# Optimization experiments

Measured on AMD Instinct MI355X. Metric: run time of the kernel, lower is better.

Reference implementation:

```python
import jax, jax.numpy as jnp
import numpy as np

B, S, H = 2, 2048, 2048
NH = 16
HD = H // NH  # 128


def setup_inputs() -> dict:
    key = jax.random.key(0)
    ks = jax.random.split(key, 6)
    sc = 0.02
    return {
        "x": jax.random.normal(ks[0], (B, S, H), dtype=jnp.float32),
        "attention_mask": jnp.zeros((B, S), dtype=jnp.float32),
        "Wq": jax.random.normal(ks[1], (H, H), dtype=jnp.float32) * sc,
        "bq": jnp.zeros((H,), dtype=jnp.float32),
        "Wk": jax.random.normal(ks[2], (H, H), dtype=jnp.float32) * sc,
        "bk": jnp.zeros((H,), dtype=jnp.float32),
        "Wv": jax.random.normal(ks[3], (H, H), dtype=jnp.float32) * sc,
        "bv": jnp.zeros((H,), dtype=jnp.float32),
        "Wo": jax.random.normal(ks[4], (H, H), dtype=jnp.float32) * sc,
        "bo": jnp.zeros((H,), dtype=jnp.float32),
    }


def reference(x, attention_mask, Wq, bq, Wk, bk, Wv, bv, Wo, bo):
    b, s, h = x.shape
    q = (x @ Wq + bq).reshape(b, s, NH, HD)
    k = (x @ Wk + bk).reshape(b, s, NH, HD)
    v = (x @ Wv + bv).reshape(b, s, NH, HD)
    scale = 1.0 / jnp.sqrt(jnp.asarray(HD, dtype=x.dtype))
    scores = jnp.einsum('bqhd,bkhd->bhqk', q, k) * scale
    scores = scores + attention_mask[:, None, None, :]
    weights = jax.nn.softmax(scores, axis=-1)
    attn = jnp.einsum('bhqk,bkhd->bqhd', weights, v).reshape(b, s, h)
    return attn @ Wo + bo
```

## Files before the change

kernel.cpp:

```cpp
#include <hip/hip_runtime.h>
#include <hip/hip_bf16.h>
#include <stdint.h>

#define BB   2
#define SS   2048
#define HHH  2048
#define NHH  16
#define HDD  128
#define MTOT 4096

typedef __bf16 bf16x8 __attribute__((ext_vector_type(8)));
typedef float  f32x4  __attribute__((ext_vector_type(4)));
typedef float  f32x16 __attribute__((ext_vector_type(16)));

#define MFMA16(a, b, c) __builtin_amdgcn_mfma_f32_16x16x32_bf16((a), (b), (c), 0, 0, 0)
#define MFMA32(a, b, c) __builtin_amdgcn_mfma_f32_32x32x16_bf16((a), (b), (c), 0, 0, 0)

__device__ __forceinline__ unsigned short f2bf(float f) {
    union { float f; unsigned u; } v; v.f = f;
    unsigned r = v.u + 0x7FFFu + ((v.u >> 16) & 1u);
    return (unsigned short)(r >> 16);
}

__device__ __forceinline__ unsigned packbf(float a, float b) {
    union { __bf16 h[2]; unsigned u; } p;
    p.h[0] = (__bf16)a; p.h[1] = (__bf16)b;
    return p.u;
}

__device__ __forceinline__ void pswap(unsigned &a, unsigned &b) {
    asm("v_permlane32_swap_b32 %0, %1" : "+v"(a), "+v"(b));
}

__device__ __forceinline__ float2 xswap(float x) {
    unsigned a = __builtin_bit_cast(unsigned, x);
    unsigned b;
    asm("v_mov_b32 %0, %1" : "=v"(b) : "v"(a));
    asm("v_permlane32_swap_b32 %0, %1" : "+v"(a), "+v"(b));
    return make_float2(__builtin_bit_cast(float, a), __builtin_bit_cast(float, b));
}

__device__ __forceinline__ void gload16(const void* src, void* lds) {
    __builtin_amdgcn_global_load_lds(
        (__attribute__((address_space(1))) void*)src,
        (__attribute__((address_space(3))) void*)lds,
        16, 0, 0);
}

__global__ void cast_f32_bf16(const float* __restrict__ in,
                              unsigned short* __restrict__ out, int n) {
    int i = (blockIdx.x * blockDim.x + threadIdx.x) * 4;
    int stride = gridDim.x * blockDim.x * 4;
    for (; i < n; i += stride) {
        float4 v = *(const float4*)(in + i);
        ushort4 o;
        o.x = f2bf(v.x); o.y = f2bf(v.y); o.z = f2bf(v.z); o.w = f2bf(v.w);
        *(ushort4*)(out + i) = o;
    }
}

__global__ void transpose_cast4(const float* __restrict__ W0, const float* __restrict__ W1,
                                const float* __restrict__ W2, const float* __restrict__ W3,
                                unsigned short* __restrict__ out) {
    const float* in = blockIdx.z == 0 ? W0 : blockIdx.z == 1 ? W1 : blockIdx.z == 2 ? W2 : W3;
    unsigned short* o = out + (size_t)blockIdx.z * ((size_t)HHH * HHH);
    __shared__ float tile[32][33];
    int c0 = blockIdx.x * 32, r0 = blockIdx.y * 32;
    int tx = threadIdx.x, ty = threadIdx.y;
    #pragma unroll
    for (int i = 0; i < 32; i += 8)
        tile[ty + i][tx] = in[(size_t)(r0 + ty + i) * HHH + c0 + tx];
    __syncthreads();
    #pragma unroll
    for (int i = 0; i < 32; i += 8)
        o[(size_t)(c0 + ty + i) * HHH + r0 + tx] = f2bf(tile[tx][ty + i]);
}

template<int MODE>
__global__ __launch_bounds__(512, 2) void gemm8_bf16(
    const unsigned short* __restrict__ A,
    const unsigned short* __restrict__ Bt,
    const float* __restrict__ bias,
    void* __restrict__ Cout,
    int M, int N, int K)
{
    __shared__ __align__(16) unsigned char sm[147456];
    const int tid = threadIdx.x;
    const int wv = tid >> 6, ln = tid & 63;
    const int g = ln >> 4, r = ln & 15;
    const int wr = wv >> 2, wc = wv & 3;

    const int bid = blockIdx.x;
    const int lb = (bid & 7) * 32 + (bid >> 3);
    const int m0 = (lb & 31) * 128;
    const int n0 = (lb >> 5) * 256;

    unsigned srcA[2]; int ldsA[2];
    #pragma unroll
    for (int j = 0; j < 2; ++j) {
        int o = j * 8192 + tid * 16;
        int row = o >> 7;
        int lg = ((o >> 4) & 7) ^ (row & 7);
        srcA[j] = (unsigned)(m0 + row) * K + lg * 8;
        ldsA[j] = o;
    }
    unsigned srcB[4]; int ldsB[4];
    #pragma unroll
    for (int j = 0; j < 4; ++j) {
        int o = j * 8192 + tid * 16;
        int row = o >> 7;
        int lg = ((o >> 4) & 7) ^ (row & 7);
        srcB[j] = (unsigned)(n0 + row) * K + lg * 8;
        ldsB[j] = 16384 + o;
    }

    f32x4 acc[4][4];
    #pragma unroll
    for (int i = 0; i < 4; ++i)
        #pragma unroll
        for (int j = 0; j < 4; ++j)
            acc[i][j] = (f32x4){0.f, 0.f, 0.f, 0.f};

    const int NT = K >> 6;

    {
        unsigned char* b0 = sm;
        unsigned char* b1 = sm + 49152;
        #pragma unroll
        for (int j = 0; j < 2; ++j) gload16(A + srcA[j], b0 + ldsA[j]);
        #pragma unroll
        for (int j = 0; j < 4; ++j) gload16(Bt + srcB[j], b0 + ldsB[j]);
        #pragma unroll
        for (int j = 0; j < 2; ++j) gload16(A + srcA[j] + 64, b1 + ldsA[j]);
        #pragma unroll
        for (int j = 0; j < 4; ++j) gload16(Bt + srcB[j] + 64, b1 + ldsB[j]);
    }
    asm volatile("s_waitcnt vmcnt(6)" ::: "memory");
    __builtin_amdgcn_s_barrier();

    int csel = 0;
    int psel = 2;
    for (int t = 0; t < NT; ++t) {
        const unsigned char* Ab = sm + csel * 49152;
        const unsigned char* Bb = Ab + 16384;
        unsigned char* Pb = sm + psel * 49152;
        const bool pre = (t + 2 < NT);
        const int ko = (t + 2) * 64;

        bf16x8 af[2][2], bf[2][2];
        #define LDA(mi, ks) (*(const bf16x8*)(Ab + (wr * 64 + (mi) * 16 + r) * 128 + \
                             ((((ks) << 2) + g) ^ ((wr * 64 + (mi) * 16 + r) & 7)) * 16))
        #define LDB(ni, ks) (*(const bf16x8*)(Bb + (wc * 64 + (ni) * 16 + r) * 128 + \
                             ((((ks) << 2) + g) ^ ((wc * 64 + (ni) * 16 + r) & 7)) * 16))

        af[0][0] = LDA(0, 0); af[0][1] = LDA(0, 1);
        af[1][0] = LDA(1, 0); af[1][1] = LDA(1, 1);
        bf[0][0] = LDB(0, 0); bf[0][1] = LDB(0, 1);
        bf[1][0] = LDB(1, 0); bf[1][1] = LDB(1, 1);
        if (pre) { gload16(Bt + srcB[0] + ko, Pb + ldsB[0]);
                   gload16(Bt + srcB[1] + ko, Pb + ldsB[1]); }
        __builtin_amdgcn_s_barrier();
        asm volatile("s_waitcnt lgkmcnt(0)" ::: "memory");
        __builtin_amdgcn_s_setprio(1);
        #pragma unroll
        for (int mi = 0; mi < 2; ++mi)
            #pragma unroll
            for (int ni = 0; ni < 2; ++ni)
                #pragma unroll
                for (int ks = 0; ks < 2; ++ks)
                    acc[mi][ni] = MFMA16(af[mi][ks], bf[ni][ks], acc[mi][ni]);
        __builtin_amdgcn_s_setprio(0);
        __builtin_amdgcn_s_barrier();

        bf[0][0] = LDB(2, 0); bf[0][1] = LDB(2, 1);
        bf[1][0] = LDB(3, 0); bf[1][1] = LDB(3, 1);
        if (pre) { gload16(Bt + srcB[2] + ko, Pb + ldsB[2]);
                   gload16(Bt + srcB[3] + ko, Pb + ldsB[3]); }
        __builtin_amdgcn_s_barrier();
        asm volatile("s_waitcnt lgkmcnt(0)" ::: "memory");
        __builtin_amdgcn_s_setprio(1);
        #pragma unroll
        for (int mi = 0; mi < 2; ++mi)
            #pragma unroll
            for (int ni = 0; ni < 2; ++ni)
                #pragma unroll
                for (int ks = 0; ks < 2; ++ks)
                    acc[mi][ni + 2] = MFMA16(af[mi][ks], bf[ni][ks], acc[mi][ni + 2]);
        __builtin_amdgcn_s_setprio(0);
        __builtin_amdgcn_s_barrier();

        af[0][0] = LDA(2, 0); af[0][1] = LDA(2, 1);
        af[1][0] = LDA(3, 0); af[1][1] = LDA(3, 1);
        if (pre) { gload16(A + srcA[0] + ko, Pb + ldsA[0]);
                   gload16(A + srcA[1] + ko, Pb + ldsA[1]); }
        __builtin_amdgcn_s_barrier();
        asm volatile("s_waitcnt lgkmcnt(0)" ::: "memory");
        __builtin_amdgcn_s_setprio(1);
        #pragma unroll
        for (int mi = 0; mi < 2; ++mi)
            #pragma unroll
            for (int ni = 0; ni < 2; ++ni)
                #pragma unroll
                for (int ks = 0; ks < 2; ++ks)
                    acc[mi + 2][ni + 2] = MFMA16(af[mi][ks], bf[ni][ks], acc[mi + 2][ni + 2]);
        __builtin_amdgcn_s_setprio(0);
        __builtin_amdgcn_s_barrier();

        bf[0][0] = LDB(0, 0); bf[0][1] = LDB(0, 1);
        bf[1][0] = LDB(1, 0); bf[1][1] = LDB(1, 1);
        __builtin_amdgcn_s_barrier();
        asm volatile("s_waitcnt lgkmcnt(0)" ::: "memory");
        __builtin_amdgcn_s_setprio(1);
        #pragma unroll
        for (int mi = 0; mi < 2; ++mi)
            #pragma unroll
            for (int ni = 0; ni < 2; ++ni)
                #pragma unroll
                for (int ks = 0; ks < 2; ++ks)
                    acc[mi + 2][ni] = MFMA16(af[mi][ks], bf[ni][ks], acc[mi + 2][ni]);
        __builtin_amdgcn_s_setprio(0);
        __builtin_amdgcn_s_barrier();

        if (pre) asm volatile("s_waitcnt vmcnt(6)" ::: "memory");
        else     asm volatile("s_waitcnt vmcnt(0)" ::: "memory");
        __builtin_amdgcn_s_barrier();

        csel = (csel == 2) ? 0 : csel + 1;
        psel = (psel == 2) ? 0 : psel + 1;
        #undef LDA
        #undef LDB
    }

    #pragma unroll
    for (int mt = 0; mt < 4; ++mt) {
        #pragma unroll
        for (int nt = 0; nt < 4; ++nt) {
            int col = n0 + wc * 64 + nt * 16 + r;
            float bvv = bias[col];
            f32x4 a = acc[mt][nt];
            int mrow = m0 + wr * 64 + mt * 16 + g * 4;
            if (MODE == 0) {
                #pragma unroll
                for (int q = 0; q < 4; ++q)
                    ((unsigned short*)Cout)[(size_t)(mrow + q) * N + col] = f2bf(a[q] + bvv);
            } else if (MODE == 2) {
                #pragma unroll
                for (int q = 0; q < 4; ++q)
                    ((float*)Cout)[(size_t)(mrow + q) * N + col] = a[q] + bvv;
            } else {
                int b = mrow >> 11, s0x = mrow & 2047;
                ushort4 o;
                o.x = f2bf(a[0] + bvv); o.y = f2bf(a[1] + bvv);
                o.z = f2bf(a[2] + bvv); o.w = f2bf(a[3] + bvv);
                *(ushort4*)((unsigned short*)Cout + ((size_t)(b * 2048 + col)) * 2048 + s0x) = o;
            }
        }
    }
}

__global__ __launch_bounds__(256, 2) void attn_fwd(
    const unsigned short* __restrict__ Q,
    const unsigned short* __restrict__ K,
    const unsigned short* __restrict__ V,
    const float* __restrict__ mask,
    unsigned short* __restrict__ O)
{
    __shared__ __align__(16) unsigned char sm[65536];
    const int tid = threadIdx.x, wv = tid >> 6, ln = tid & 63;
    const int hi = ln >> 5, qr = ln & 31;

    const int bid = blockIdx.x;
    const int lb = (bid & 7) * 64 + (bid >> 3);
    const int qb = lb & 15;
    const int bh = lb >> 4;
    const int h = bh & 15, b = bh >> 4;

    const size_t rowQ0 = (size_t)(b * 2048 + qb * 128 + wv * 32);
    const float SCL2 = 0.08838834764831845f * 1.4426950408889634f;
    const float L2E  = 1.4426950408889634f;

    unsigned srcK[4], srcV[4];
    int ldsK[4], ldsV[4];
    #pragma unroll
    for (int i = 0; i < 4; ++i) {
        int ch = wv * 4 + i;
        int o = ch * 1024 + ln * 16;
        { int row = o >> 8; int gl = ((o >> 4) & 15) ^ (row & 7);
          srcK[i] = (unsigned)((b * 2048 + row) * 2048 + h * 128 + gl * 8);
          ldsK[i] = ch * 1024; }
        { int d = o >> 7; int gl = ((o >> 4) & 7) ^ (d & 7);
          srcV[i] = (unsigned)((b * 2048 + h * 128 + d) * 2048 + gl * 8);
          ldsV[i] = 16384 + ch * 1024; }
    }

    #pragma unroll
    for (int i = 0; i < 4; ++i) {
        gload16(K + srcK[i], sm + ldsK[i]);
        gload16(V + srcV[i], sm + ldsV[i]);
    }

    bf16x8 qf[8];
    #pragma unroll
    for (int ks = 0; ks < 8; ++ks)
        qf[ks] = *(const bf16x8*)(Q + (rowQ0 + qr) * 2048 + h * 128 + ks * 16 + hi * 8);

    f32x16 acc[4];
    #pragma unroll
    for (int i = 0; i < 4; ++i)
        #pragma unroll
        for (int j = 0; j < 16; ++j)
            acc[i][j] = 0.f;
    float mr = -3.0e38f, lr = 0.f;

    const float* mb = mask + b * 2048;
    int cur = 0;
    __syncthreads();

    for (int kb = 0; kb < SS; kb += 64) {
        if (kb + 64 < SS) {
            const unsigned char* dst = sm + (cur ^ 1) * 32768;
            int ko = (kb + 64) * 2048;
            #pragma unroll
            for (int i = 0; i < 4; ++i) {
                gload16(K + srcK[i] + ko, (void*)(dst + ldsK[i]));
                gload16(V + srcV[i] + (kb + 64), (void*)(dst + ldsV[i]));
            }
        }
        const unsigned char* Kt = sm + cur * 32768;
        const unsigned char* Vt = Kt + 16384;

        f32x4 mk[2][4];
        #pragma unroll
        for (int kb2 = 0; kb2 < 2; ++kb2)
            #pragma unroll
            for (int rg = 0; rg < 4; ++rg)
                mk[kb2][rg] = *(const f32x4*)(mb + kb + kb2 * 32 + rg * 8 + hi * 4);

        f32x16 sf0, sf1;
        #pragma unroll
        for (int j = 0; j < 16; ++j) { sf0[j] = 0.f; sf1[j] = 0.f; }
        __builtin_amdgcn_s_setprio(1);
        #pragma unroll
        for (int ks = 0; ks < 8; ++ks) {
            int row0 = qr, row1 = 32 + qr;
            int s0 = ((2 * ks + hi) ^ (row0 & 7));
            int s1 = ((2 * ks + hi) ^ (row1 & 7));
            bf16x8 kf0 = *(const bf16x8*)(Kt + row0 * 256 + s0 * 16);
            bf16x8 kf1 = *(const bf16x8*)(Kt + row1 * 256 + s1 * 16);
            sf0 = MFMA32(kf0, qf[ks], sf0);
            sf1 = MFMA32(kf1, qf[ks], sf1);
        }
        __builtin_amdgcn_s_setprio(0);

        float sv[2][16];
        #pragma unroll
        for (int reg = 0; reg < 16; ++reg) {
            sv[0][reg] = sf0[reg] * SCL2 + mk[0][reg >> 2][reg & 3] * L2E;
            sv[1][reg] = sf1[reg] * SCL2 + mk[1][reg >> 2][reg & 3] * L2E;
        }

        float mx[8];
        #pragma unroll
        for (int j = 0; j < 8; ++j)
            mx[j] = fmaxf(fmaxf(sv[0][2*j], sv[0][2*j+1]),
                          fmaxf(sv[1][2*j], sv[1][2*j+1]));
        float m01 = fmaxf(fmaxf(fmaxf(mx[0], mx[1]), fmaxf(mx[2], mx[3])),
                          fmaxf(fmaxf(mx[4], mx[5]), fmaxf(mx[6], mx[7])));
        float2 mp = xswap(m01);
        float mt = fmaxf(mp.x, mp.y);

        float alpha = 1.f;
        int allskip = __all(mt <= mr + 8.f);
        if (!allskip) {
            float nm = fmaxf(mr, mt);
            alpha = __builtin_amdgcn_exp2f(mr - nm);
            mr = nm;
            #pragma unroll
            for (int dblk = 0; dblk < 4; ++dblk)
                #pragma unroll
                for (int reg = 0; reg < 16; ++reg)
                    acc[dblk][reg] *= alpha;
        }

        float s0 = 0.f, s1 = 0.f, s2 = 0.f, s3 = 0.f;
        #pragma unroll
        for (int kb2 = 0; kb2 < 2; ++kb2)
            #pragma unroll
            for (int reg = 0; reg < 16; reg += 4) {
                float p0 = __builtin_amdgcn_exp2f(sv[kb2][reg + 0] - mr);
                float p1 = __builtin_amdgcn_exp2f(sv[kb2][reg + 1] - mr);
                float p2 = __builtin_amdgcn_exp2f(sv[kb2][reg + 2] - mr);
                float p3 = __builtin_amdgcn_exp2f(sv[kb2][reg + 3] - mr);
                sv[kb2][reg + 0] = p0; sv[kb2][reg + 1] = p1;
                sv[kb2][reg + 2] = p2; sv[kb2][reg + 3] = p3;
                s0 += p0; s1 += p1; s2 += p2; s3 += p3;
            }
        float rsl = (s0 + s1) + (s2 + s3);
        float2 rp = xswap(rsl);
        float rs = rp.x + rp.y;
        lr = lr * alpha + rs;

        bf16x8 pfr[4];
        #pragma unroll
        for (int kb16 = 0; kb16 < 4; ++kb16) {
            const int kb2 = kb16 >> 1, i2 = kb16 & 1;
            float* pv = sv[kb2];
            unsigned W00 = packbf(pv[(2*i2+0)*4 + 0], pv[(2*i2+0)*4 + 1]);
            unsigned W01 = packbf(pv[(2*i2+0)*4 + 2], pv[(2*i2+0)*4 + 3]);
            unsigned W10 = packbf(pv[(2*i2+1)*4 + 0], pv[(2*i2+1)*4 + 1]);
            unsigned W11 = packbf(pv[(2*i2+1)*4 + 2], pv[(2*i2+1)*4 + 3]);
            pswap(W00, W10);
            pswap(W01, W11);
            union { unsigned w[4]; bf16x8 v; } u;
            u.w[0] = W00; u.w[1] = W01; u.w[2] = W10; u.w[3] = W11;
            pfr[kb16] = u.v;
        }

        __builtin_amdgcn_s_setprio(1);
        #pragma unroll
        for (int dblk = 0; dblk < 4; ++dblk) {
            int d = dblk * 32 + qr;
            f32x16 a = acc[dblk];
            #pragma unroll
            for (int kb16 = 0; kb16 < 4; ++kb16) {
                int s = ((2 * kb16 + hi) ^ (d & 7));
                bf16x8 vf = *(const bf16x8*)(Vt + d * 128 + s * 16);
                a = MFMA32(vf, pfr[kb16], a);
            }
            acc[dblk] = a;
        }
        __builtin_amdgcn_s_setprio(0);

        __syncthreads();
        cur ^= 1;
    }

    float linv = 1.f / lr;
    unsigned short* orow = O + (rowQ0 + qr) * 2048 + h * 128;
    #pragma unroll
    for (int dblk = 0; dblk < 4; ++dblk)
        #pragma unroll
        for (int rg = 0; rg < 4; ++rg) {
            float v0 = acc[dblk][rg * 4 + 0] * linv;
            float v1 = acc[dblk][rg * 4 + 1] * linv;
            float v2 = acc[dblk][rg * 4 + 2] * linv;
            float v3 = acc[dblk][rg * 4 + 3] * linv;
            uint2 o;
            o.x = packbf(v0, v1);
            o.y = packbf(v2, v3);
            *(uint2*)(orow + dblk * 32 + rg * 8 + hi * 4) = o;
        }
}

extern "C" void kernel_launch(void* const* d_in, const int* in_sizes, int n_in,
                              void* d_out, int out_size, void* d_ws, size_t ws_size,
                              hipStream_t stream)
{
    (void)in_sizes; (void)n_in; (void)out_size; (void)ws_size;
    const float* x    = (const float*)d_in[0];
    const float* mask = (const float*)d_in[1];
    const float* Wq   = (const float*)d_in[2];
    const float* bq   = (const float*)d_in[3];
    const float* Wk   = (const float*)d_in[4];
    const float* bk   = (const float*)d_in[5];
    const float* Wv   = (const float*)d_in[6];
    const float* bv   = (const float*)d_in[7];
    const float* Wo   = (const float*)d_in[8];
    const float* bo   = (const float*)d_in[9];
    float* out = (float*)d_out;

    char* ws = (char*)d_ws;
    unsigned short* xb  = (unsigned short*)(ws);
    unsigned short* Wqt = (unsigned short*)(ws + (16u << 20));
    unsigned short* Wkt = (unsigned short*)(ws + (24u << 20));
    unsigned short* Wvt = (unsigned short*)(ws + (32u << 20));
    unsigned short* Wot = (unsigned short*)(ws + (40u << 20));
    unsigned short* Qb  = (unsigned short*)(ws + (48u << 20));
    unsigned short* Kb  = (unsigned short*)(ws + (64u << 20));
    unsigned short* Vtb = (unsigned short*)(ws + (80u << 20));
    unsigned short* Ab  = (unsigned short*)(ws + (16u << 20));

    cast_f32_bf16<<<2048, 256, 0, stream>>>(x, xb, MTOT * HHH);
    transpose_cast4<<<dim3(64, 64, 4), dim3(32, 8), 0, stream>>>(Wq, Wk, Wv, Wo, Wqt);

    gemm8_bf16<0><<<256, 512, 0, stream>>>(xb, Wqt, bq, Qb,  MTOT, HHH, HHH);
    gemm8_bf16<0><<<256, 512, 0, stream>>>(xb, Wkt, bk, Kb,  MTOT, HHH, HHH);
    gemm8_bf16<1><<<256, 512, 0, stream>>>(xb, Wvt, bv, Vtb, MTOT, HHH, HHH);

    attn_fwd<<<BB * NHH * (SS / 128), 256, 0, stream>>>(Qb, Kb, Vtb, mask, Ab);

    gemm8_bf16<2><<<256, 512, 0, stream>>>(Ab, Wot, bo, out, MTOT, HHH, HHH);
}
```

Measured before the change: 290.6 us.

## Split attention KV range across two blocks and merge partials in combine kernel

Splits the attention over keys into two halves (split-K / flash-decoding style). Each half is handled by its own block with smaller 32-key tiles and half the LDS, which allows higher occupancy via launch bounds of 4. Each block writes a normalized partial output plus its running max and sum. A new combine kernel then rescales and merges the two partials into the final attention output. This targets low occupancy and too few blocks in the attention kernel, at the cost of extra partial-output traffic, an added launch, and a second bf16 rounding step.

```diff
diff --git a/kernel.cpp b/kernel.cpp
--- a/kernel.cpp
+++ b/kernel.cpp
@@ -45,6 +45,13 @@
         (__attribute__((address_space(1))) void*)src,
         (__attribute__((address_space(3))) void*)lds,
         16, 0, 0);
+}
+
+__device__ __forceinline__ float bflo(unsigned w) {
+    return __builtin_bit_cast(float, w << 16);
+}
+__device__ __forceinline__ float bfhi(unsigned w) {
+    return __builtin_bit_cast(float, w & 0xffff0000u);
 }
 
 __global__ void cast_f32_bf16(const float* __restrict__ in,
@@ -258,43 +265,48 @@
     }
 }
 
-__global__ __launch_bounds__(256, 2) void attn_fwd(
+__global__ __launch_bounds__(256, 4) void attn_fwd(
     const unsigned short* __restrict__ Q,
     const unsigned short* __restrict__ K,
     const unsigned short* __restrict__ V,
     const float* __restrict__ mask,
-    unsigned short* __restrict__ O)
+    unsigned short* __restrict__ P0,
+    unsigned short* __restrict__ P1,
+    float2* __restrict__ ML0,
+    float2* __restrict__ ML1)
 {
-    __shared__ __align__(16) unsigned char sm[65536];
+    __shared__ __align__(16) unsigned char sm[32768];
     const int tid = threadIdx.x, wv = tid >> 6, ln = tid & 63;
     const int hi = ln >> 5, qr = ln & 31;
 
     const int bid = blockIdx.x;
-    const int lb = (bid & 7) * 64 + (bid >> 3);
-    const int qb = lb & 15;
-    const int bh = lb >> 4;
+    const int lb = (bid & 7) * 128 + (bid >> 3);
+    const int sp = lb & 1;
+    const int qb = (lb >> 1) & 15;
+    const int bh = lb >> 5;
     const int h = bh & 15, b = bh >> 4;
 
     const size_t rowQ0 = (size_t)(b * 2048 + qb * 128 + wv * 32);
+    const int kbase = sp * 1024;
     const float SCL2 = 0.08838834764831845f * 1.4426950408889634f;
     const float L2E  = 1.4426950408889634f;
 
-    unsigned srcK[4], srcV[4];
-    int ldsK[4], ldsV[4];
-    #pragma unroll
-    for (int i = 0; i < 4; ++i) {
-        int ch = wv * 4 + i;
+    unsigned srcK[2], srcV[2];
+    int ldsK[2], ldsV[2];
+    #pragma unroll
+    for (int i = 0; i < 2; ++i) {
+        int ch = wv * 2 + i;
         int o = ch * 1024 + ln * 16;
         { int row = o >> 8; int gl = ((o >> 4) & 15) ^ (row & 7);
-          srcK[i] = (unsigned)((b * 2048 + row) * 2048 + h * 128 + gl * 8);
-          ldsK[i] = ch * 1024; }
-        { int d = o >> 7; int gl = ((o >> 4) & 7) ^ (d & 7);
-          srcV[i] = (unsigned)((b * 2048 + h * 128 + d) * 2048 + gl * 8);
-          ldsV[i] = 16384 + ch * 1024; }
-    }
-
-    #pragma unroll
-    for (int i = 0; i < 4; ++i) {
+          srcK[i] = (unsigned)((b * 2048 + kbase + row) * 2048 + h * 128 + gl * 8);
+          ldsK[i] = o; }
+        { int d = o >> 6; int gl = ((o >> 4) & 3) ^ (d & 3);
+          srcV[i] = (unsigned)((b * 2048 + h * 128 + d) * 2048 + kbase + gl * 8);
+          ldsV[i] = 8192 + o; }
+    }
+
+    #pragma unroll
+    for (int i = 0; i < 2; ++i) {
         gload16(K + srcK[i], sm + ldsK[i]);
         gload16(V + srcV[i], sm + ldsV[i]);
     }
@@ -312,58 +324,49 @@
             acc[i][j] = 0.f;
     float mr = -3.0e38f, lr = 0.f;
 
-    const float* mb = mask + b * 2048;
+    const float* mb = mask + b * 2048 + kbase;
     int cur = 0;
     __syncthreads();
 
-    for (int kb = 0; kb < SS; kb += 64) {
-        if (kb + 64 < SS) {
-            const unsigned char* dst = sm + (cur ^ 1) * 32768;
-            int ko = (kb + 64) * 2048;
-            #pragma unroll
-            for (int i = 0; i < 4; ++i) {
-                gload16(K + srcK[i] + ko, (void*)(dst + ldsK[i]));
-                gload16(V + srcV[i] + (kb + 64), (void*)(dst + ldsV[i]));
+    for (int t = 0; t < 32; ++t) {
+        const int kb = t * 32;
+        if (t + 1 < 32) {
+            unsigned char* dst = sm + (cur ^ 1) * 16384;
+            #pragma unroll
+            for (int i = 0; i < 2; ++i) {
+                gload16(K + srcK[i] + (kb + 32) * 2048, dst + ldsK[i]);
+                gload16(V + srcV[i] + (kb + 32), dst + ldsV[i]);
             }
         }
-        const unsigned char* Kt = sm + cur * 32768;
-        const unsigned char* Vt = Kt + 16384;
-
-        f32x4 mk[2][4];
-        #pragma unroll
-        for (int kb2 = 0; kb2 < 2; ++kb2)
-            #pragma unroll
-            for (int rg = 0; rg < 4; ++rg)
-                mk[kb2][rg] = *(const f32x4*)(mb + kb + kb2 * 32 + rg * 8 + hi * 4);
-
-        f32x16 sf0, sf1;
-        #pragma unroll
-        for (int j = 0; j < 16; ++j) { sf0[j] = 0.f; sf1[j] = 0.f; }
+        const unsigned char* Kt = sm + cur * 16384;
+        const unsigned char* Vt = Kt + 8192;
+
+        f32x4 mk[4];
+        #pragma unroll
+        for (int rg = 0; rg < 4; ++rg)
+            mk[rg] = *(const f32x4*)(mb + kb + rg * 8 + hi * 4);
+
+        f32x16 sf;
+        #pragma unroll
+        for (int j = 0; j < 16; ++j) sf[j] = 0.f;
         __builtin_amdgcn_s_setprio(1);
         #pragma unroll
         for (int ks = 0; ks < 8; ++ks) {
-            int row0 = qr, row1 = 32 + qr;
-            int s0 = ((2 * ks + hi) ^ (row0 & 7));
-            int s1 = ((2 * ks + hi) ^ (row1 & 7));
-            bf16x8 kf0 = *(const bf16x8*)(Kt + row0 * 256 + s0 * 16);
-            bf16x8 kf1 = *(const bf16x8*)(Kt + row1 * 256 + s1 * 16);
-            sf0 = MFMA32(kf0, qf[ks], sf0);
-            sf1 = MFMA32(kf1, qf[ks], sf1);
+            int s0 = (2 * ks + hi) ^ (qr & 7);
+            bf16x8 kf = *(const bf16x8*)(Kt + qr * 256 + s0 * 16);
+            sf = MFMA32(kf, qf[ks], sf);
         }
         __builtin_amdgcn_s_setprio(0);
 
-        float sv[2][16];
-        #pragma unroll
-        for (int reg = 0; reg < 16; ++reg) {
-            sv[0][reg] = sf0[reg] * SCL2 + mk[0][reg >> 2][reg & 3] * L2E;
-            sv[1][reg] = sf1[reg] * SCL2 + mk[1][reg >> 2][reg & 3] * L2E;
-        }
+        float sv[16];
+        #pragma unroll
+        for (int reg = 0; reg < 16; ++reg)
+            sv[reg] = sf[reg] * SCL2 + mk[reg >> 2][reg & 3] * L2E;
 
         float mx[8];
         #pragma unroll
         for (int j = 0; j < 8; ++j)
-            mx[j] = fmaxf(fmaxf(sv[0][2*j], sv[0][2*j+1]),
-                          fmaxf(sv[1][2*j], sv[1][2*j+1]));
+            mx[j] = fmaxf(sv[2 * j], sv[2 * j + 1]);
         float m01 = fmaxf(fmaxf(fmaxf(mx[0], mx[1]), fmaxf(mx[2], mx[3])),
                           fmaxf(fmaxf(mx[4], mx[5]), fmaxf(mx[6], mx[7])));
         float2 mp = xswap(m01);
@@ -384,31 +387,27 @@
 
         float s0 = 0.f, s1 = 0.f, s2 = 0.f, s3 = 0.f;
         #pragma unroll
-        for (int kb2 = 0; kb2 < 2; ++kb2)
-            #pragma unroll
-            for (int reg = 0; reg < 16; reg += 4) {
-                float p0 = __builtin_amdgcn_exp2f(sv[kb2][reg + 0] - mr);
-                float p1 = __builtin_amdgcn_exp2f(sv[kb2][reg + 1] - mr);
-                float p2 = __builtin_amdgcn_exp2f(sv[kb2][reg + 2] - mr);
-                float p3 = __builtin_amdgcn_exp2f(sv[kb2][reg + 3] - mr);
-                sv[kb2][reg + 0] = p0; sv[kb2][reg + 1] = p1;
-                sv[kb2][reg + 2] = p2; sv[kb2][reg + 3] = p3;
-                s0 += p0; s1 += p1; s2 += p2; s3 += p3;
-            }
+        for (int reg = 0; reg < 16; reg += 4) {
+            float p0 = __builtin_amdgcn_exp2f(sv[reg + 0] - mr);
+            float p1 = __builtin_amdgcn_exp2f(sv[reg + 1] - mr);
+            float p2 = __builtin_amdgcn_exp2f(sv[reg + 2] - mr);
+            float p3 = __builtin_amdgcn_exp2f(sv[reg + 3] - mr);
+            sv[reg + 0] = p0; sv[reg + 1] = p1;
+            sv[reg + 2] = p2; sv[reg + 3] = p3;
+            s0 += p0; s1 += p1; s2 += p2; s3 += p3;
+        }
         float rsl = (s0 + s1) + (s2 + s3);
         float2 rp = xswap(rsl);
         float rs = rp.x + rp.y;
         lr = lr * alpha + rs;
 
-        bf16x8 pfr[4];
-        #pragma unroll
-        for (int kb16 = 0; kb16 < 4; ++kb16) {
-            const int kb2 = kb16 >> 1, i2 = kb16 & 1;
-            float* pv = sv[kb2];
-            unsigned W00 = packbf(pv[(2*i2+0)*4 + 0], pv[(2*i2+0)*4 + 1]);
-            unsigned W01 = packbf(pv[(2*i2+0)*4 + 2], pv[(2*i2+0)*4 + 3]);
-            unsigned W10 = packbf(pv[(2*i2+1)*4 + 0], pv[(2*i2+1)*4 + 1]);
-            unsigned W11 = packbf(pv[(2*i2+1)*4 + 2], pv[(2*i2+1)*4 + 3]);
+        bf16x8 pfr[2];
+        #pragma unroll
+        for (int kb16 = 0; kb16 < 2; ++kb16) {
+            unsigned W00 = packbf(sv[(2*kb16+0)*4 + 0], sv[(2*kb16+0)*4 + 1]);
+            unsigned W01 = packbf(sv[(2*kb16+0)*4 + 2], sv[(2*kb16+0)*4 + 3]);
+            unsigned W10 = packbf(sv[(2*kb16+1)*4 + 0], sv[(2*kb16+1)*4 + 1]);
+            unsigned W11 = packbf(sv[(2*kb16+1)*4 + 2], sv[(2*kb16+1)*4 + 3]);
             pswap(W00, W10);
             pswap(W01, W11);
             union { unsigned w[4]; bf16x8 v; } u;
@@ -422,9 +421,9 @@
             int d = dblk * 32 + qr;
             f32x16 a = acc[dblk];
             #pragma unroll
-            for (int kb16 = 0; kb16 < 4; ++kb16) {
-                int s = ((2 * kb16 + hi) ^ (d & 7));
-                bf16x8 vf = *(const bf16x8*)(Vt + d * 128 + s * 16);
+            for (int kb16 = 0; kb16 < 2; ++kb16) {
+                int s = (2 * kb16 + hi) ^ (d & 3);
+                bf16x8 vf = *(const bf16x8*)(Vt + d * 64 + s * 16);
                 a = MFMA32(vf, pfr[kb16], a);
             }
             acc[dblk] = a;
@@ -436,7 +435,8 @@
     }
 
     float linv = 1.f / lr;
-    unsigned short* orow = O + (rowQ0 + qr) * 2048 + h * 128;
+    unsigned short* Pp = sp ? P1 : P0;
+    unsigned short* orow = Pp + (rowQ0 + qr) * 2048 + h * 128;
     #pragma unroll
     for (int dblk = 0; dblk < 4; ++dblk)
         #pragma unroll
@@ -450,6 +450,37 @@
             o.y = packbf(v2, v3);
             *(uint2*)(orow + dblk * 32 + rg * 8 + hi * 4) = o;
         }
+    if (hi == 0) {
+        float2* ml = sp ? ML1 : ML0;
+        ml[(rowQ0 + qr) * 16 + h] = make_float2(mr, lr);
+    }
+}
+
+__global__ void attn_combine(const unsigned short* __restrict__ P0,
+                             const unsigned short* __restrict__ P1,
+                             const float2* __restrict__ ML0,
+                             const float2* __restrict__ ML1,
+                             unsigned short* __restrict__ O)
+{
+    int t = blockIdx.x * 256 + threadIdx.x;
+    int base = t * 8;
+    int row = base >> 11;
+    int h = (base & 2047) >> 7;
+    float2 a = ML0[row * 16 + h];
+    float2 c = ML1[row * 16 + h];
+    float M = fmaxf(a.x, c.x);
+    float w0 = __builtin_amdgcn_exp2f(a.x - M) * a.y;
+    float w1 = __builtin_amdgcn_exp2f(c.x - M) * c.y;
+    float inv = 1.f / (w0 + w1);
+    w0 *= inv; w1 *= inv;
+    uint4 u0 = *(const uint4*)(P0 + base);
+    uint4 u1 = *(const uint4*)(P1 + base);
+    uint4 o;
+    o.x = packbf(w0 * bflo(u0.x) + w1 * bflo(u1.x), w0 * bfhi(u0.x) + w1 * bfhi(u1.x));
+    o.y = packbf(w0 * bflo(u0.y) + w1 * bflo(u1.y), w0 * bfhi(u0.y) + w1 * bfhi(u1.y));
+    o.z = packbf(w0 * bflo(u0.z) + w1 * bflo(u1.z), w0 * bfhi(u0.z) + w1 * bfhi(u1.z));
+    o.w = packbf(w0 * bflo(u0.w) + w1 * bflo(u1.w), w0 * bfhi(u0.w) + w1 * bfhi(u1.w));
+    *(uint4*)(O + base) = o;
 }
 
 extern "C" void kernel_launch(void* const* d_in, const int* in_sizes, int n_in,
@@ -478,7 +509,11 @@
     unsigned short* Qb  = (unsigned short*)(ws + (48u << 20));
     unsigned short* Kb  = (unsigned short*)(ws + (64u << 20));
     unsigned short* Vtb = (unsigned short*)(ws + (80u << 20));
-    unsigned short* Ab  = (unsigned short*)(ws + (16u << 20));
+    unsigned short* Op0 = (unsigned short*)(ws);
+    unsigned short* Op1 = (unsigned short*)(ws + (16u << 20));
+    float2*         ML0 = (float2*)(ws + (32u << 20));
+    float2*         ML1 = (float2*)(ws + (36u << 20));
+    unsigned short* Ab  = (unsigned short*)(ws + (48u << 20));
 
     cast_f32_bf16<<<2048, 256, 0, stream>>>(x, xb, MTOT * HHH);
     transpose_cast4<<<dim3(64, 64, 4), dim3(32, 8), 0, stream>>>(Wq, Wk, Wv, Wo, Wqt);
@@ -487,7 +522,8 @@
     gemm8_bf16<0><<<256, 512, 0, stream>>>(xb, Wkt, bk, Kb,  MTOT, HHH, HHH);
     gemm8_bf16<1><<<256, 512, 0, stream>>>(xb, Wvt, bv, Vtb, MTOT, HHH, HHH);
 
-    attn_fwd<<<BB * NHH * (SS / 128), 256, 0, stream>>>(Qb, Kb, Vtb, mask, Ab);
+    attn_fwd<<<1024, 256, 0, stream>>>(Qb, Kb, Vtb, mask, Op0, Op1, ML0, ML1);
+    attn_combine<<<(MTOT * HHH) / (256 * 8), 256, 0, stream>>>(Op0, Op1, ML0, ML1, Ab);
 
     gemm8_bf16<2><<<256, 512, 0, stream>>>(Ab, Wot, bo, out, MTOT, HHH, HHH);
 }
```

After: 403.8 us. +39.0%, slower.

## Restructure GEMM inner loop to two phases and pipeline attention K/V loads

Applied to the files above, without the earlier changes.

The GEMM main loop now loads all four B fragments at once and runs two MFMA phases instead of four, cutting the number of barriers per k-tile while holding more B registers. Attention switches from double-buffered loads issued at the top of each iteration to loads issued after a barrier at the end of the iteration with explicit vmcnt waits. The mask is pre-scaled by log2(e) in a small kernel and staged into LDS, so the per-element multiply and global mask reads leave the inner loop. LDS use per attention block grows and register pressure in the GEMM rises, which may lower occupancy.

```diff
diff --git a/kernel.cpp b/kernel.cpp
--- a/kernel.cpp
+++ b/kernel.cpp
@@ -57,6 +57,11 @@
         o.x = f2bf(v.x); o.y = f2bf(v.y); o.z = f2bf(v.z); o.w = f2bf(v.w);
         *(ushort4*)(out + i) = o;
     }
+}
+
+__global__ void scale_mask(const float* __restrict__ in, float* __restrict__ out) {
+    int i = blockIdx.x * 256 + threadIdx.x;
+    out[i] = in[i] * 1.4426950408889634f;
 }
 
 __global__ void transpose_cast4(const float* __restrict__ W0, const float* __restrict__ W1,
@@ -147,7 +152,7 @@
         const bool pre = (t + 2 < NT);
         const int ko = (t + 2) * 64;
 
-        bf16x8 af[2][2], bf[2][2];
+        bf16x8 af[2][2], bfr[4][2];
         #define LDA(mi, ks) (*(const bf16x8*)(Ab + (wr * 64 + (mi) * 16 + r) * 128 + \
                              ((((ks) << 2) + g) ^ ((wr * 64 + (mi) * 16 + r) & 7)) * 16))
         #define LDB(ni, ks) (*(const bf16x8*)(Bb + (wc * 64 + (ni) * 16 + r) * 128 + \
@@ -155,71 +160,43 @@
 
         af[0][0] = LDA(0, 0); af[0][1] = LDA(0, 1);
         af[1][0] = LDA(1, 0); af[1][1] = LDA(1, 1);
-        bf[0][0] = LDB(0, 0); bf[0][1] = LDB(0, 1);
-        bf[1][0] = LDB(1, 0); bf[1][1] = LDB(1, 1);
+        #pragma unroll
+        for (int ni = 0; ni < 4; ++ni) {
+            bfr[ni][0] = LDB(ni, 0);
+            bfr[ni][1] = LDB(ni, 1);
+        }
         if (pre) { gload16(Bt + srcB[0] + ko, Pb + ldsB[0]);
-                   gload16(Bt + srcB[1] + ko, Pb + ldsB[1]); }
+                   gload16(Bt + srcB[1] + ko, Pb + ldsB[1]);
+                   gload16(Bt + srcB[2] + ko, Pb + ldsB[2]); }
         __builtin_amdgcn_s_barrier();
         asm volatile("s_waitcnt lgkmcnt(0)" ::: "memory");
         __builtin_amdgcn_s_setprio(1);
         #pragma unroll
         for (int mi = 0; mi < 2; ++mi)
             #pragma unroll
-            for (int ni = 0; ni < 2; ++ni)
+            for (int ni = 0; ni < 4; ++ni)
                 #pragma unroll
                 for (int ks = 0; ks < 2; ++ks)
-                    acc[mi][ni] = MFMA16(af[mi][ks], bf[ni][ks], acc[mi][ni]);
+                    acc[mi][ni] = MFMA16(af[mi][ks], bfr[ni][ks], acc[mi][ni]);
         __builtin_amdgcn_s_setprio(0);
         __builtin_amdgcn_s_barrier();
 
-        bf[0][0] = LDB(2, 0); bf[0][1] = LDB(2, 1);
-        bf[1][0] = LDB(3, 0); bf[1][1] = LDB(3, 1);
-        if (pre) { gload16(Bt + srcB[2] + ko, Pb + ldsB[2]);
-                   gload16(Bt + srcB[3] + ko, Pb + ldsB[3]); }
+        af[0][0] = LDA(2, 0); af[0][1] = LDA(2, 1);
+        af[1][0] = LDA(3, 0); af[1][1] = LDA(3, 1);
+        if (pre) { gload16(Bt + srcB[3] + ko, Pb + ldsB[3]);
+                   gload16(A + srcA[0] + ko, Pb + ldsA[0]);
+                   gload16(A + srcA[1] + ko, Pb + ldsA[1]); }
         __builtin_amdgcn_s_barrier();
         asm volatile("s_waitcnt lgkmcnt(0)" ::: "memory");
         __builtin_amdgcn_s_setprio(1);
         #pragma unroll
         for (int mi = 0; mi < 2; ++mi)
             #pragma unroll
-            for (int ni = 0; ni < 2; ++ni)
+            for (int ni = 0; ni < 4; ++ni)
                 #pragma unroll
                 for (int ks = 0; ks < 2; ++ks)
-                    acc[mi][ni + 2] = MFMA16(af[mi][ks], bf[ni][ks], acc[mi][ni + 2]);
+                    acc[mi + 2][ni] = MFMA16(af[mi][ks], bfr[ni][ks], acc[mi + 2][ni]);
         __builtin_amdgcn_s_setprio(0);
-        __builtin_amdgcn_s_barrier();
-
-        af[0][0] = LDA(2, 0); af[0][1] = LDA(2, 1);
-        af[1][0] = LDA(3, 0); af[1][1] = LDA(3, 1);
-        if (pre) { gload16(A + srcA[0] + ko, Pb + ldsA[0]);
-                   gload16(A + srcA[1] + ko, Pb + ldsA[1]); }
-        __builtin_amdgcn_s_barrier();
-        asm volatile("s_waitcnt lgkmcnt(0)" ::: "memory");
-        __builtin_amdgcn_s_setprio(1);
-        #pragma unroll
-        for (int mi = 0; mi < 2; ++mi)
-            #pragma unroll
-            for (int ni = 0; ni < 2; ++ni)
-                #pragma unroll
-                for (int ks = 0; ks < 2; ++ks)
-                    acc[mi + 2][ni + 2] = MFMA16(af[mi][ks], bf[ni][ks], acc[mi + 2][ni + 2]);
-        __builtin_amdgcn_s_setprio(0);
-        __builtin_amdgcn_s_barrier();
-
-        bf[0][0] = LDB(0, 0); bf[0][1] = LDB(0, 1);
-        bf[1][0] = LDB(1, 0); bf[1][1] = LDB(1, 1);
-        __builtin_amdgcn_s_barrier();
-        asm volatile("s_waitcnt lgkmcnt(0)" ::: "memory");
-        __builtin_amdgcn_s_setprio(1);
-        #pragma unroll
-        for (int mi = 0; mi < 2; ++mi)
-            #pragma unroll
-            for (int ni = 0; ni < 2; ++ni)
-                #pragma unroll
-                for (int ks = 0; ks < 2; ++ks)
-                    acc[mi + 2][ni] = MFMA16(af[mi][ks], bf[ni][ks], acc[mi + 2][ni]);
-        __builtin_amdgcn_s_setprio(0);
-        __builtin_amdgcn_s_barrier();
 
         if (pre) asm volatile("s_waitcnt vmcnt(6)" ::: "memory");
         else     asm volatile("s_waitcnt vmcnt(0)" ::: "memory");
@@ -262,10 +239,10 @@
     const unsigned short* __restrict__ Q,
     const unsigned short* __restrict__ K,
     const unsigned short* __restrict__ V,
-    const float* __restrict__ mask,
+    const float* __restrict__ maskl2,
     unsigned short* __restrict__ O)
 {
-    __shared__ __align__(16) unsigned char sm[65536];
+    __shared__ __align__(16) unsigned char sm[73728];
     const int tid = threadIdx.x, wv = tid >> 6, ln = tid & 63;
     const int hi = ln >> 5, qr = ln & 31;
 
@@ -277,7 +254,6 @@
 
     const size_t rowQ0 = (size_t)(b * 2048 + qb * 128 + wv * 32);
     const float SCL2 = 0.08838834764831845f * 1.4426950408889634f;
-    const float L2E  = 1.4426950408889634f;
 
     unsigned srcK[4], srcV[4];
     int ldsK[4], ldsV[4];
@@ -287,17 +263,24 @@
         int o = ch * 1024 + ln * 16;
         { int row = o >> 8; int gl = ((o >> 4) & 15) ^ (row & 7);
           srcK[i] = (unsigned)((b * 2048 + row) * 2048 + h * 128 + gl * 8);
-          ldsK[i] = ch * 1024; }
+          ldsK[i] = o; }
         { int d = o >> 7; int gl = ((o >> 4) & 7) ^ (d & 7);
           srcV[i] = (unsigned)((b * 2048 + h * 128 + d) * 2048 + gl * 8);
-          ldsV[i] = 16384 + ch * 1024; }
-    }
-
-    #pragma unroll
-    for (int i = 0; i < 4; ++i) {
-        gload16(K + srcK[i], sm + ldsK[i]);
-        gload16(V + srcV[i], sm + ldsV[i]);
-    }
+          ldsV[i] = 16384 + o; }
+    }
+
+    #define STAGE(t, base) { \
+        _Pragma("unroll") \
+        for (int i = 0; i < 4; ++i) { \
+            gload16(K + srcK[i] + (unsigned)(t) * (64u * 2048u), sm + (base) + ldsK[i]); \
+            gload16(V + srcV[i] + (unsigned)(t) * 64u, sm + (base) + ldsV[i]); \
+        } }
+
+    #pragma unroll
+    for (int i = 0; i < 2; ++i)
+        gload16(maskl2 + b * 2048 + wv * 512 + i * 256 + ln * 4,
+                sm + 65536 + wv * 2048 + i * 1024);
+    STAGE(0, 0); STAGE(1, 32768);
 
     bf16x8 qf[8];
     #pragma unroll
@@ -312,21 +295,13 @@
             acc[i][j] = 0.f;
     float mr = -3.0e38f, lr = 0.f;
 
-    const float* mb = mask + b * 2048;
-    int cur = 0;
-    __syncthreads();
-
-    for (int kb = 0; kb < SS; kb += 64) {
-        if (kb + 64 < SS) {
-            const unsigned char* dst = sm + (cur ^ 1) * 32768;
-            int ko = (kb + 64) * 2048;
-            #pragma unroll
-            for (int i = 0; i < 4; ++i) {
-                gload16(K + srcK[i] + ko, (void*)(dst + ldsK[i]));
-                gload16(V + srcV[i] + (kb + 64), (void*)(dst + ldsV[i]));
-            }
-        }
-        const unsigned char* Kt = sm + cur * 32768;
+    const float* ml = (const float*)(sm + 65536);
+
+    asm volatile("s_waitcnt vmcnt(8)" ::: "memory");
+    __builtin_amdgcn_s_barrier();
+
+    for (int t = 0; t < 32; ++t) {
+        const unsigned char* Kt = sm + (t & 1) * 32768;
         const unsigned char* Vt = Kt + 16384;
 
         f32x4 mk[2][4];
@@ -334,7 +309,7 @@
         for (int kb2 = 0; kb2 < 2; ++kb2)
             #pragma unroll
             for (int rg = 0; rg < 4; ++rg)
-                mk[kb2][rg] = *(const f32x4*)(mb + kb + kb2 * 32 + rg * 8 + hi * 4);
+                mk[kb2][rg] = *(const f32x4*)(ml + t * 64 + kb2 * 32 + rg * 8 + hi * 4);
 
         f32x16 sf0, sf1;
         #pragma unroll
@@ -355,8 +330,8 @@
         float sv[2][16];
         #pragma unroll
         for (int reg = 0; reg < 16; ++reg) {
-            sv[0][reg] = sf0[reg] * SCL2 + mk[0][reg >> 2][reg & 3] * L2E;
-            sv[1][reg] = sf1[reg] * SCL2 + mk[1][reg >> 2][reg & 3] * L2E;
+            sv[0][reg] = sf0[reg] * SCL2 + mk[0][reg >> 2][reg & 3];
+            sv[1][reg] = sf1[reg] * SCL2 + mk[1][reg >> 2][reg & 3];
         }
 
         float mx[8];
@@ -431,8 +406,14 @@
         }
         __builtin_amdgcn_s_setprio(0);
 
-        __syncthreads();
-        cur ^= 1;
+        __builtin_amdgcn_s_barrier();
+        if (t + 2 < 32) {
+            STAGE(t + 2, (t & 1) * 32768);
+            asm volatile("s_waitcnt vmcnt(8)" ::: "memory");
+        } else {
+            asm volatile("s_waitcnt vmcnt(0)" ::: "memory");
+        }
+        __builtin_amdgcn_s_barrier();
     }
 
     float linv = 1.f / lr;
@@ -450,6 +431,7 @@
             o.y = packbf(v2, v3);
             *(uint2*)(orow + dblk * 32 + rg * 8 + hi * 4) = o;
         }
+    #undef STAGE
 }
 
 extern "C" void kernel_launch(void* const* d_in, const int* in_sizes, int n_in,
@@ -479,6 +461,7 @@
     unsigned short* Kb  = (unsigned short*)(ws + (64u << 20));
     unsigned short* Vtb = (unsigned short*)(ws + (80u << 20));
     unsigned short* Ab  = (unsigned short*)(ws + (16u << 20));
+    float*          mkl = (float*)(ws + (32u << 20));
 
     cast_f32_bf16<<<2048, 256, 0, stream>>>(x, xb, MTOT * HHH);
     transpose_cast4<<<dim3(64, 64, 4), dim3(32, 8), 0, stream>>>(Wq, Wk, Wv, Wo, Wqt);
@@ -487,7 +470,8 @@
     gemm8_bf16<0><<<256, 512, 0, stream>>>(xb, Wkt, bk, Kb,  MTOT, HHH, HHH);
     gemm8_bf16<1><<<256, 512, 0, stream>>>(xb, Wvt, bv, Vtb, MTOT, HHH, HHH);
 
-    attn_fwd<<<BB * NHH * (SS / 128), 256, 0, stream>>>(Qb, Kb, Vtb, mask, Ab);
+    scale_mask<<<(BB * SS) / 256, 256, 0, stream>>>(mask, mkl);
+    attn_fwd<<<512, 256, 0, stream>>>(Qb, Kb, Vtb, mkl, Ab);
 
     gemm8_bf16<2><<<256, 512, 0, stream>>>(Ab, Wot, bo, out, MTOT, HHH, HHH);
 }
```

Result: faster. 276.2 us (-4.9%).
